# Kernel optimization log

Measured on AMD Instinct MI355X. Metric: run time of the kernel, lower is better.

The kernel has to match this reference:

```python
import jax, jax.numpy as jnp
import numpy as np

B, T, NE, NH, HD = 4, 1024, 768, 12, 64
CURV = 0.0
EPS = 1e-6
LN_EPS = 1e-5
ROPE_BASE = 10000.0


def project(x, k):
    # Lift Euclidean vector onto Lorentz hyperboloid with curvature K = exp(k):
    # time coord t = sqrt(K + ||x||^2) so that <lx, lx>_L = -K.
    K = jnp.exp(k)
    t = jnp.sqrt(K + jnp.sum(x * x, axis=-1, keepdims=True))
    return jnp.concatenate([t, x], axis=-1)


def lorentz_distance(lq, lk, k):
    # lq, lk: (B, H, T, D+1); k: (1, H, 1, 1) log-curvature.
    # d = sqrt(K) * arccosh(clamp(-<q,k>_L / K, 1+eps))
    K = jnp.exp(k)
    inner = (jnp.einsum('bhid,bhjd->bhij', lq[..., 1:], lk[..., 1:])
             - jnp.einsum('bhi,bhj->bhij', lq[..., 0], lk[..., 0]))
    c = jnp.clip(-inner / K, 1.0 + EPS, None)
    return jnp.sqrt(K) * jnp.arccosh(c)


def lorentz_norm(x):
    # sqrt(|<x,x>_L|) with <x,x>_L = -x0^2 + ||xs||^2  (keepdim)
    inner = -x[..., 0:1] ** 2 + jnp.sum(x[..., 1:] ** 2, axis=-1, keepdims=True)
    return jnp.sqrt(jnp.clip(-inner, EPS, None))


def rotary_tables():
    inv_freq = 1.0 / (ROPE_BASE ** (np.arange(0, HD, 2, dtype=np.float32) / HD))
    t = np.arange(T, dtype=np.float32)
    freqs = np.outer(t, inv_freq)  # (T, HD/2)
    cos = jnp.asarray(np.cos(freqs))[None, :, None, :]  # (1,T,1,HD/2)
    sin = jnp.asarray(np.sin(freqs))[None, :, None, :]
    return cos, sin


def apply_rotary(x, cos, sin):
    # x: (B, T, H, HD)
    x1, x2 = x[..., : HD // 2], x[..., HD // 2:]
    return jnp.concatenate([x1 * cos + x2 * sin, -x1 * sin + x2 * cos], axis=-1)


def layernorm(y, g, b):
    m = jnp.mean(y, axis=-1, keepdims=True)
    v = jnp.mean((y - m) ** 2, axis=-1, keepdims=True)
    return (y - m) / jnp.sqrt(v + LN_EPS) * g + b


def setup_inputs() -> dict:
    key = jax.random.key(0)
    ks = jax.random.split(key, 8)
    s = 0.02
    return {
        'x': jax.random.normal(ks[0], (B, T, NE), dtype=jnp.float32),
        'block_curvature': jnp.asarray(CURV, dtype=jnp.float32),
        'mlp_curvature': jnp.asarray(CURV, dtype=jnp.float32),
        'attn_curvatures': jnp.ones((1, NH, 1, 1), dtype=jnp.float32) * CURV,
        'qkv_w': jax.random.normal(ks[1], (3 * NE, NE + 1), dtype=jnp.float32) * s,
        'attn_proj_w': jax.random.normal(ks[2], (NE, (HD + 1) * NH), dtype=jnp.float32) * s,
        'attn_proj_b': jnp.zeros((NE,), dtype=jnp.float32),
        'mlp_expand_w': jax.random.normal(ks[3], (4 * NE + 3, NE + 1), dtype=jnp.float32) * s,
        'mlp_expand_b': jnp.zeros((4 * NE + 3,), dtype=jnp.float32),
        'mlp_shrink_w': jax.random.normal(ks[4], (NE, 4 * (NE + 1)), dtype=jnp.float32) * s,
        'mlp_shrink_b': jnp.zeros((NE,), dtype=jnp.float32),
        'ln_g': jnp.ones((NE,), dtype=jnp.float32),
        'ln_b': jnp.zeros((NE,), dtype=jnp.float32),
    }


def reference(x, block_curvature, mlp_curvature, attn_curvatures, qkv_w,
              attn_proj_w, attn_proj_b, mlp_expand_w, mlp_expand_b,
              mlp_shrink_w, mlp_shrink_b, ln_g, ln_b):
    cos, sin = rotary_tables()
    causal_bias = jnp.where(
        jnp.triu(jnp.ones((T, T), dtype=bool), k=1), -jnp.inf, 0.0).astype(jnp.float32)

    def block_norm(lx):
        return project(layernorm(lx[..., 1:], ln_g, ln_b), block_curvature)

    def attn(lx):
        qkv = lx @ qkv_w.T  # (B, T, 3*NE)
        q, k, v = jnp.split(qkv, 3, axis=-1)
        q = apply_rotary(q.reshape(B, T, NH, HD), cos, sin)
        k = apply_rotary(k.reshape(B, T, NH, HD), cos, sin)
        v = v.reshape(B, T, NH, HD)
        lq = project(q.transpose(0, 2, 1, 3), attn_curvatures)  # (B,H,T,HD+1)
        lk = project(k.transpose(0, 2, 1, 3), attn_curvatures)
        lv = project(v.transpose(0, 2, 1, 3), attn_curvatures)
        dis = lorentz_distance(lq, lk, attn_curvatures)  # (B,H,T,T)
        aw = jax.nn.softmax(-dis + causal_bias, axis=-1)
        a = jnp.einsum('bhij,bhjd->bhid', aw, lv)  # (B,H,T,HD+1)
        a = a * jnp.sqrt(jnp.exp(attn_curvatures)) / lorentz_norm(a)
        a = a.transpose(0, 2, 1, 3).reshape(B, T, NH * (HD + 1))
        a = a @ attn_proj_w.T + attn_proj_b
        return project(a, block_curvature)

    def mlp(lx):
        h = lx @ mlp_expand_w.T + mlp_expand_b  # (B,T,4*NE+3)
        h = project(h, mlp_curvature)[..., 1:]  # drop time coord back to 4*NE+3
        h = jax.nn.gelu(h, approximate=False)
        h = project(h, mlp_curvature)  # (B,T,4*(NE+1))
        h = h @ mlp_shrink_w.T + mlp_shrink_b
        return project(h, block_curvature)

    def skip(lx, f_lx):
        return project(lx[..., 1:] + f_lx[..., 1:], block_curvature)

    lx = project(x, block_curvature)  # (B,T,NE+1)
    lx = skip(lx, attn(block_norm(lx)))
    lx = skip(lx, mlp(block_norm(lx)))
    return lx
```

## Files before the change

### kernel.cpp

```cpp
#include <hip/hip_runtime.h>
#include <cmath>

typedef unsigned short ushort_t;
typedef __attribute__((ext_vector_type(8))) short short8;
typedef __attribute__((ext_vector_type(4))) float floatx4;

#define NH    12
#define T     1024
#define ROWS  4096
#define NE    768
#define KPA   832
#define KPB   3136
#define NEXP  3200
#define HEXP  3075
#define NSPLIT 3

__device__ __forceinline__ ushort_t f2bf(float f) {
  union { float f; unsigned u; } v; v.f = f;
  unsigned r = v.u + 0x7fffu + ((v.u >> 16) & 1u);
  return (ushort_t)(r >> 16);
}
__device__ __forceinline__ ushort_t f2bf_trunc(float f) {
  union { float f; unsigned u; } v; v.f = f;
  return (ushort_t)(v.u >> 16);
}
__device__ __forceinline__ float bf2f(ushort_t b) {
  union { unsigned u; float f; } v; v.u = ((unsigned)b) << 16;
  return v.f;
}
__device__ __forceinline__ float blk_reduce_sum(float v, float* sm) {
  #pragma unroll
  for (int o = 32; o > 0; o >>= 1) v += __shfl_xor(v, o, 64);
  int lane = threadIdx.x & 63, w = threadIdx.x >> 6;
  __syncthreads();
  if (lane == 0) sm[w] = v;
  __syncthreads();
  return sm[0] + sm[1] + sm[2] + sm[3];
}
__device__ __forceinline__ float red16_sum(float v) {
  #pragma unroll
  for (int o = 1; o < 16; o <<= 1) v += __shfl_xor(v, o, 64);
  return v;
}

#define NB_A 7488
#define NB_B 2496
#define NB_C 10400
#define NB_D 9408
#define NB_E 16
__device__ __forceinline__ void cvt_elem(ushort_t* __restrict__ dst,
                                         const float* __restrict__ src,
                                         int idx, int srcRows, int srcK, int dstK) {
  int r = idx / dstK, c = idx - r * dstK;
  dst[idx] = (r < srcRows && c < srcK) ? f2bf(src[(size_t)r * srcK + c]) : (ushort_t)0;
}
__global__ __launch_bounds__(256) void prep_kernel(
    ushort_t* __restrict__ qkv_wb, const float* __restrict__ qkvw,
    ushort_t* __restrict__ proj_wb, const float* __restrict__ projw,
    ushort_t* __restrict__ exp_wb, const float* __restrict__ expw,
    ushort_t* __restrict__ shr_wb, const float* __restrict__ shrw,
    ushort_t* __restrict__ aout_bf,
    const float* __restrict__ xin, const float* __restrict__ g,
    const float* __restrict__ bb, const float* __restrict__ curv,
    ushort_t* __restrict__ lnp) {
  __shared__ float sm[4];
  int blk = blockIdx.x;
  int tid = threadIdx.x;
  if (blk < NB_A) {
    cvt_elem(qkv_wb, qkvw, blk * 256 + tid, 2304, 769, KPA);
  } else if (blk < NB_A + NB_B) {
    cvt_elem(proj_wb, projw, (blk - NB_A) * 256 + tid, 768, 780, KPA);
  } else if (blk < NB_A + NB_B + NB_C) {
    cvt_elem(exp_wb, expw, (blk - NB_A - NB_B) * 256 + tid, HEXP, 769, KPA);
  } else if (blk < NB_A + NB_B + NB_C + NB_D) {
    cvt_elem(shr_wb, shrw, (blk - NB_A - NB_B - NB_C) * 256 + tid, 768, 3076, KPB);
  } else if (blk < NB_A + NB_B + NB_C + NB_D + NB_E) {
    int r = (blk - NB_A - NB_B - NB_C - NB_D) * 256 + tid;
    ushort_t* p = aout_bf + (size_t)r * KPA + 780;
    #pragma unroll
    for (int j = 0; j < KPA - 780; ++j) p[j] = 0;
  } else {
    const int row = blk - (NB_A + NB_B + NB_C + NB_D + NB_E);
    const float* xr = xin + (size_t)row * NE;
    float xv[3];
    float s = 0.f, ss = 0.f;
    #pragma unroll
    for (int i = 0; i < 3; ++i) {
      xv[i] = xr[tid + 256 * i];
      s += xv[i]; ss += xv[i] * xv[i];
    }
    s = blk_reduce_sum(s, sm);
    ss = blk_reduce_sum(ss, sm);
    float mean = s * (1.f / 768.f);
    float var = ss * (1.f / 768.f) - mean * mean;
    float rstd = rsqrtf(var + 1e-5f);
    float yv[3]; float ys = 0.f;
    #pragma unroll
    for (int i = 0; i < 3; ++i) {
      int c = tid + 256 * i;
      yv[i] = (xv[i] - mean) * rstd * g[c] + bb[c];
      ys += yv[i] * yv[i];
    }
    ys = blk_reduce_sum(ys, sm);
    float tc = sqrtf(expf(curv[0]) + ys);
    ushort_t* orow = lnp + (size_t)row * KPA;
    #pragma unroll
    for (int i = 0; i < 3; ++i) orow[1 + tid + 256 * i] = f2bf(yv[i]);
    if (tid == 0) orow[0] = f2bf(tc);
    if (tid < KPA - 769) orow[769 + tid] = 0;
  }
}

__global__ __launch_bounds__(256) void gemm_bf16(
    const ushort_t* __restrict__ A, int lda,
    const ushort_t* __restrict__ W, int ldw,
    void* __restrict__ Cout, int ldc,
    int nkTot, int cpt,
    const float* __restrict__ bias, int biasN,
    const float* __restrict__ res, int ldres,
    int outMode, void* __restrict__ Cp) {
  __shared__ ushort_t As[2][128 * 64];
  __shared__ ushort_t Bs[2][128 * 64];
  const int tid = threadIdx.x;
  const int w = tid >> 6, lane = tid & 63;
  const int rowBase = (int)blockIdx.y << 7;
  const int colBase = (int)blockIdx.x << 7;
  const int wm = (w & 1) * 64, wn = (w >> 1) * 64;
  const int lm = lane & 15, quad = lane >> 4;
  const int p0 = quad ^ (lm & 7);

  floatx4 acc[4][4];
  #pragma unroll
  for (int i = 0; i < 4; ++i)
    #pragma unroll
    for (int j = 0; j < 4; ++j) {
      floatx4 z = {0.f, 0.f, 0.f, 0.f};
      acc[i][j] = z;
    }

  const int kt0 = (int)blockIdx.z * cpt;
  const int kt1 = min(nkTot, kt0 + cpt);

  auto stage = [&](int kt, int bsel) {
    #pragma unroll
    for (int j = 0; j < 4; ++j) {
      int ci = j * 256 + tid;
      int r = ci >> 3;
      int g = (ci & 7) ^ (r & 7);
      const ushort_t* ga = A + (size_t)(rowBase + r) * lda + kt * 64 + g * 8;
      const ushort_t* gb = W + (size_t)(colBase + r) * ldw + kt * 64 + g * 8;
      __builtin_amdgcn_global_load_lds(
          (const __attribute__((address_space(1))) void*)ga,
          (__attribute__((address_space(3))) void*)&As[bsel][(j * 256 + w * 64) * 8],
          16, 0, 0);
      __builtin_amdgcn_global_load_lds(
          (const __attribute__((address_space(1))) void*)gb,
          (__attribute__((address_space(3))) void*)&Bs[bsel][(j * 256 + w * 64) * 8],
          16, 0, 0);
    }
  };

  stage(kt0, 0);
  asm volatile("s_waitcnt vmcnt(0)" ::: "memory");
  __builtin_amdgcn_s_barrier();
  __builtin_amdgcn_sched_barrier(0);

  int cur = 0;
  for (int kt = kt0; kt < kt1; ++kt) {
    const bool hasNext = (kt + 1 < kt1);
    if (hasNext) stage(kt + 1, cur ^ 1);

    #pragma unroll
    for (int s = 0; s < 2; ++s) {
      const int ps = s ? (p0 ^ 4) : p0;
      short8 af[4], bfr[4];
      #pragma unroll
      for (int i = 0; i < 4; ++i) {
        af[i]  = *(const short8*)&As[cur][(wm + i * 16 + lm) * 64 + ps * 8];
        bfr[i] = *(const short8*)&Bs[cur][(wn + i * 16 + lm) * 64 + ps * 8];
      }
      #pragma unroll
      for (int i = 0; i < 4; ++i)
        #pragma unroll
        for (int jn = 0; jn < 4; ++jn)
          acc[i][jn] = __builtin_amdgcn_mfma_f32_16x16x32_bf16(
              af[i], bfr[jn], acc[i][jn], 0, 0, 0);
    }

    if (hasNext) {
      asm volatile("s_waitcnt vmcnt(0)" ::: "memory");
      __builtin_amdgcn_s_barrier();
      __builtin_amdgcn_sched_barrier(0);
    }
    cur ^= 1;
  }

  if (gridDim.z > 1) {
    ushort_t* dst = (ushort_t*)Cp + (size_t)blockIdx.z * ROWS * ldc;
    #pragma unroll
    for (int i = 0; i < 4; ++i)
      #pragma unroll
      for (int jn = 0; jn < 4; ++jn) {
        const int col = colBase + wn + jn * 16 + lm;
        #pragma unroll
        for (int rg = 0; rg < 4; ++rg) {
          const int row = rowBase + wm + i * 16 + quad * 4 + rg;
          dst[(size_t)row * ldc + col] = f2bf(acc[i][jn][rg]);
        }
      }
  } else if (outMode == 1) {
    ushort_t* C = (ushort_t*)Cout;
    #pragma unroll
    for (int i = 0; i < 4; ++i)
      #pragma unroll
      for (int jn = 0; jn < 4; ++jn) {
        const int col = colBase + wn + jn * 16 + lm;
        const float bv = bias ? ((col < biasN) ? bias[col] : 0.f) : 0.f;
        #pragma unroll
        for (int rg = 0; rg < 4; ++rg) {
          const int row = rowBase + wm + i * 16 + quad * 4 + rg;
          C[(size_t)row * ldc + col] = f2bf(acc[i][jn][rg] + bv);
        }
      }
  } else {
    float* C = (float*)Cout;
    #pragma unroll
    for (int i = 0; i < 4; ++i)
      #pragma unroll
      for (int jn = 0; jn < 4; ++jn) {
        const int col = colBase + wn + jn * 16 + lm;
        const float bv = bias ? ((col < biasN) ? bias[col] : 0.f) : 0.f;
        #pragma unroll
        for (int rg = 0; rg < 4; ++rg) {
          const int row = rowBase + wm + i * 16 + quad * 4 + rg;
          float o = acc[i][jn][rg] + bv;
          if (res) o += res[(size_t)row * ldres + col];
          C[(size_t)row * ldc + col] = o;
        }
      }
  }
}

__global__ __launch_bounds__(256) void rope_project(
    const ushort_t* __restrict__ qkv, const float* __restrict__ ac,
    ushort_t* __restrict__ qb, ushort_t* __restrict__ kb, ushort_t* __restrict__ vtb,
    float* __restrict__ q0, float* __restrict__ k0, float* __restrict__ v0) {
  int gid = blockIdx.x * 4 + (threadIdx.x >> 6);
  int lane = threadIdx.x & 63;
  int h = gid % NH;
  int bt = gid / NH;
  int t = bt & (T - 1);
  int b = bt >> 10;
  size_t base = (size_t)bt * 2304 + h * 64;
  float qv = bf2f(qkv[base + lane]);
  float kv = bf2f(qkv[base + 768 + lane]);
  float vv = bf2f(qkv[base + 1536 + lane]);
  int f = lane & 31;
  float ang = (float)t * __builtin_amdgcn_exp2f(-(float)f * 0.4152410118661534f);
  float sn, cs;
  sincosf(ang, &sn, &cs);
  float qp = __shfl(qv, lane ^ 32, 64);
  float kp = __shfl(kv, lane ^ 32, 64);
  float qr = (lane < 32) ? (qv * cs + qp * sn) : (-qp * sn + qv * cs);
  float kr = (lane < 32) ? (kv * cs + kp * sn) : (-kp * sn + kv * cs);
  float Kh = expf(ac[h]);
  float sq = qr * qr, sk = kr * kr, sv = vv * vv;
  #pragma unroll
  for (int o = 32; o > 0; o >>= 1) {
    sq += __shfl_xor(sq, o, 64);
    sk += __shfl_xor(sk, o, 64);
    sv += __shfl_xor(sv, o, 64);
  }
  size_t idx = ((size_t)(b * NH + h) * T + t);
  qb[idx * 64 + lane] = f2bf(qr);
  kb[idx * 64 + lane] = f2bf(kr);
  vtb[(size_t)(b * NH + h) * (64 * T) + (size_t)lane * T + t] = f2bf(vv);
  if (lane == 0) {
    q0[idx] = sqrtf(Kh + sq);
    k0[idx] = sqrtf(Kh + sk);
    v0[idx] = sqrtf(Kh + sv);
  }
}

__global__ __launch_bounds__(512, 4) void attn_kernel(
    const ushort_t* __restrict__ qb, const ushort_t* __restrict__ kb,
    const ushort_t* __restrict__ vtb,
    const float* __restrict__ q0, const float* __restrict__ k0,
    const float* __restrict__ v0,
    const float* __restrict__ ac,
    ushort_t* __restrict__ Opart, float* __restrict__ lpart,
    float* __restrict__ a0part) {
  __shared__ ushort_t Qs[128 * 64];
  __shared__ ushort_t Ks[2][64 * 64];
  __shared__ ushort_t Vts[2][64 * 64];
  __shared__ ushort_t Ps[128 * 72];

  const int sIdx = blockIdx.x;
  const int qtile = (int)gridDim.y - 1 - (int)blockIdx.y;
  const int bh = blockIdx.z;
  const int h = bh % NH;
  const int qt0 = qtile * 128;
  const int tid = threadIdx.x;
  const int w = tid >> 6, lane = tid & 63;
  const int lm = lane & 15, quad = lane >> 4;
  const int wm = w * 16;
  const int sw = lm & 7;

  const int n = 2 * qtile + 2;
  const int kbeg = (n * sIdx) / NSPLIT;
  const int kend = (n * (sIdx + 1)) / NSPLIT;
  const size_t pb = (size_t)(sIdx * 48 + bh) * T;

  if (kbeg >= kend) {
    #pragma unroll
    for (int r = 0; r < 4; ++r) {
      const int i = qt0 + wm + quad * 4 + r;
      ushort_t* orow = Opart + (pb + i) * 64;
      #pragma unroll
      for (int nt = 0; nt < 4; ++nt) orow[nt * 16 + lm] = 0;
      if (lm == 0) { lpart[pb + i] = 0.f; a0part[pb + i] = 0.f; }
    }
    return;
  }

  const float Kh = expf(ac[h]);
  const float sqrtK = sqrtf(Kh);
  const float invK = 1.0f / Kh;
  const float nsK = -sqrtK;
  const bool k1 = (Kh == 1.0f);

  {
    const ushort_t* qtp = qb + ((size_t)bh * T + qt0) * 64;
    #pragma unroll
    for (int j = 0; j < 2; ++j) {
      int ci = j * 512 + tid;
      int r = ci >> 3;
      int clog = ((ci & 7) ^ (r & 7)) * 8;
      __builtin_amdgcn_global_load_lds(
          (const __attribute__((address_space(1))) void*)(qtp + r * 64 + clog),
          (__attribute__((address_space(3))) void*)&Qs[(j * 8 + w) * 512],
          16, 0, 0);
    }
  }
  const ushort_t* kbase = kb + (size_t)bh * T * 64;
  const ushort_t* vbh = vtb + (size_t)bh * (64 * T);
  const float* k0row = k0 + (size_t)bh * T;
  const float* v0row = v0 + (size_t)bh * T;
  const int ldr = tid >> 3;
  const int ldcs = ((tid & 7) ^ (ldr & 7)) * 8;
  {
    const int j0 = kbeg * 64;
    __builtin_amdgcn_global_load_lds(
        (const __attribute__((address_space(1))) void*)(kbase + (size_t)(j0 + ldr) * 64 + ldcs),
        (__attribute__((address_space(3))) void*)&Ks[0][w * 512], 16, 0, 0);
    __builtin_amdgcn_global_load_lds(
        (const __attribute__((address_space(1))) void*)(vbh + (size_t)ldr * T + j0 + ldcs),
        (__attribute__((address_space(3))) void*)&Vts[0][w * 512], 16, 0, 0);
  }
  float k0n[4], v0n[4];
  #pragma unroll
  for (int jt = 0; jt < 4; ++jt) {
    k0n[jt] = k0row[kbeg * 64 + jt * 16 + lm];
    v0n[jt] = v0row[kbeg * 64 + jt * 16 + lm];
  }
  float q0rv[4];
  #pragma unroll
  for (int r = 0; r < 4; ++r)
    q0rv[r] = q0[(size_t)bh * T + qt0 + wm + quad * 4 + r];

  asm volatile("s_waitcnt vmcnt(0)" ::: "memory");
  __builtin_amdgcn_s_barrier();
  __builtin_amdgcn_sched_barrier(0);

  const short8 qf0 = *(const short8*)&Qs[(wm + lm) * 64 + ((0 + quad) ^ sw) * 8];
  const short8 qf1 = *(const short8*)&Qs[(wm + lm) * 64 + ((4 + quad) ^ sw) * 8];

  float lsum[4], a0r[4];
  floatx4 oacc[4];
  #pragma unroll
  for (int r = 0; r < 4; ++r) { lsum[r] = 0.f; a0r[r] = 0.f; }
  #pragma unroll
  for (int nt = 0; nt < 4; ++nt) { floatx4 z = {0.f,0.f,0.f,0.f}; oacc[nt] = z; }

  int cur = 0;
  for (int kt = kbeg; kt < kend; ++kt) {
    const bool hasNext = (kt + 1 < kend);
    float k0i[4], v0v[4];
    #pragma unroll
    for (int jt = 0; jt < 4; ++jt) { k0i[jt] = k0n[jt] * invK; v0v[jt] = v0n[jt]; }

    if (hasNext) {
      const int j0n = (kt + 1) * 64;
      __builtin_amdgcn_global_load_lds(
          (const __attribute__((address_space(1))) void*)(kbase + (size_t)(j0n + ldr) * 64 + ldcs),
          (__attribute__((address_space(3))) void*)&Ks[cur ^ 1][w * 512], 16, 0, 0);
      __builtin_amdgcn_global_load_lds(
          (const __attribute__((address_space(1))) void*)(vbh + (size_t)ldr * T + j0n + ldcs),
          (__attribute__((address_space(3))) void*)&Vts[cur ^ 1][w * 512], 16, 0, 0);
      #pragma unroll
      for (int jt = 0; jt < 4; ++jt) {
        k0n[jt] = k0row[j0n + jt * 16 + lm];
        v0n[jt] = v0row[j0n + jt * 16 + lm];
      }
    }

    const int j0 = kt * 64;
    const ushort_t* Kc = Ks[cur];
    const ushort_t* Vc = Vts[cur];

    floatx4 sacc[4];
    #pragma unroll
    for (int jt = 0; jt < 4; ++jt) {
      const int krow = jt * 16 + lm;
      short8 kf0 = *(const short8*)&Kc[krow * 64 + ((0 + quad) ^ sw) * 8];
      short8 kf1 = *(const short8*)&Kc[krow * 64 + ((4 + quad) ^ sw) * 8];
      floatx4 z = {0.f, 0.f, 0.f, 0.f};
      z = __builtin_amdgcn_mfma_f32_16x16x32_bf16(qf0, kf0, z, 0, 0, 0);
      z = __builtin_amdgcn_mfma_f32_16x16x32_bf16(qf1, kf1, z, 0, 0, 0);
      sacc[jt] = z;
    }

    const bool maskT = (kt >= 2 * qtile);
    if (k1) {
      #pragma unroll
      for (int r = 0; r < 4; ++r) {
        const int i = qt0 + wm + quad * 4 + r;
        float ls = 0.f, a0s = 0.f;
        #pragma unroll
        for (int jt = 0; jt < 4; ++jt) {
          float c = fmaf(-invK, sacc[jt][r], q0rv[r] * k0i[jt]);
          c = fmaxf(c, 1.000001f);
          float p = c - sqrtf(fmaf(c, c, -1.f));
          if (maskT && (j0 + jt * 16 + lm > i)) p = 0.f;
          ushort_t pb2 = f2bf_trunc(p);
          Ps[(wm + quad * 4 + r) * 72 + jt * 16 + lm] = pb2;
          float pf = bf2f(pb2);
          ls += pf;
          a0s = fmaf(pf, v0v[jt], a0s);
        }
        lsum[r] += ls;
        a0r[r] += a0s;
      }
    } else {
      #pragma unroll
      for (int r = 0; r < 4; ++r) {
        const int i = qt0 + wm + quad * 4 + r;
        float ls = 0.f, a0s = 0.f;
        #pragma unroll
        for (int jt = 0; jt < 4; ++jt) {
          float c = fmaf(-invK, sacc[jt][r], q0rv[r] * k0i[jt]);
          c = fmaxf(c, 1.000001f);
          float z = c + sqrtf(fmaf(c, c, -1.f));
          float p = __builtin_amdgcn_exp2f(nsK * __builtin_amdgcn_logf(z));
          if (maskT && (j0 + jt * 16 + lm > i)) p = 0.f;
          ushort_t pb2 = f2bf_trunc(p);
          Ps[(wm + quad * 4 + r) * 72 + jt * 16 + lm] = pb2;
          float pf = bf2f(pb2);
          ls += pf;
          a0s = fmaf(pf, v0v[jt], a0s);
        }
        lsum[r] += ls;
        a0r[r] += a0s;
      }
    }

    short8 pf0 = *(const short8*)&Ps[(wm + lm) * 72 + quad * 8];
    short8 pf1 = *(const short8*)&Ps[(wm + lm) * 72 + 32 + quad * 8];
    #pragma unroll
    for (int nt = 0; nt < 4; ++nt) {
      const int vrow = nt * 16 + lm;
      short8 vf0 = *(const short8*)&Vc[vrow * 64 + ((0 + quad) ^ sw) * 8];
      short8 vf1 = *(const short8*)&Vc[vrow * 64 + ((4 + quad) ^ sw) * 8];
      oacc[nt] = __builtin_amdgcn_mfma_f32_16x16x32_bf16(pf0, vf0, oacc[nt], 0, 0, 0);
      oacc[nt] = __builtin_amdgcn_mfma_f32_16x16x32_bf16(pf1, vf1, oacc[nt], 0, 0, 0);
    }

    if (hasNext) {
      asm volatile("s_waitcnt vmcnt(0)" ::: "memory");
      __builtin_amdgcn_s_barrier();
      __builtin_amdgcn_sched_barrier(0);
    }
    cur ^= 1;
  }

  #pragma unroll
  for (int r = 0; r < 4; ++r) {
    float lf = red16_sum(lsum[r]);
    float a0f = red16_sum(a0r[r]);
    const int i = qt0 + wm + quad * 4 + r;
    ushort_t* orow = Opart + (pb + i) * 64;
    #pragma unroll
    for (int nt = 0; nt < 4; ++nt) orow[nt * 16 + lm] = f2bf(oacc[nt][r]);
    if (lm == 0) { lpart[pb + i] = lf; a0part[pb + i] = a0f; }
  }
}

__global__ __launch_bounds__(256) void attn_combine(
    const ushort_t* __restrict__ Opart, const float* __restrict__ lpart,
    const float* __restrict__ a0part,
    const float* __restrict__ ac, ushort_t* __restrict__ aout) {
  const int widx = blockIdx.x * 4 + (threadIdx.x >> 6);
  const int lane = threadIdx.x & 63;
  const int bh = widx >> 10;
  const int t = widx & 1023;
  const int h = bh % NH, b = bh / NH;
  float L = 0.f, A0 = 0.f, O = 0.f;
  #pragma unroll
  for (int sp = 0; sp < NSPLIT; ++sp) {
    const size_t r = (size_t)(sp * 48 + bh) * T + t;
    L += lpart[r];
    A0 += a0part[r];
    O += bf2f(Opart[r * 64 + lane]);
  }
  const float invl = 1.f / L;
  float av = O * invl;
  float ssq = av * av;
  #pragma unroll
  for (int o = 32; o > 0; o >>= 1) ssq += __shfl_xor(ssq, o, 64);
  float a0n = A0 * invl;
  float nsq = fmaxf(a0n * a0n - ssq, 1e-6f);
  float Kh = expf(ac[h]);
  float scale = sqrtf(Kh) * rsqrtf(nsq);
  ushort_t* orow = aout + (size_t)(b * T + t) * KPA + h * 65;
  orow[1 + lane] = f2bf(av * scale);
  if (lane == 0) orow[0] = f2bf(a0n * scale);
}

__global__ __launch_bounds__(256) void gelu_project(
    const ushort_t* __restrict__ hsrc, const float* __restrict__ curv,
    ushort_t* __restrict__ hp) {
  __shared__ float sm[4];
  const int row = blockIdx.x;
  const int tid = threadIdx.x;
  const ushort_t* hr = hsrc + (size_t)row * NEXP;
  float gv[13];
  float ss = 0.f;
  #pragma unroll
  for (int i = 0; i < 13; ++i) {
    int c = tid + 256 * i;
    float xx = (c < HEXP) ? bf2f(hr[c]) : 0.f;
    float gg = 0.5f * xx * (1.f + erff(xx * 0.70710678118654752f));
    gv[i] = gg; ss += gg * gg;
  }
  ss = blk_reduce_sum(ss, sm);
  float tc = sqrtf(expf(curv[0]) + ss);
  ushort_t* orow = hp + (size_t)row * KPB;
  #pragma unroll
  for (int i = 0; i < 13; ++i) {
    int c = tid + 256 * i;
    if (c < HEXP) orow[1 + c] = f2bf(gv[i]);
  }
  if (tid == 0) orow[0] = f2bf(tc);
  if (tid < KPB - (HEXP + 1)) orow[HEXP + 1 + tid] = 0;
}

__global__ __launch_bounds__(256) void reduce_ln_project(
    const ushort_t* __restrict__ Cp, int nsplit,
    const float* __restrict__ bias, const float* __restrict__ res,
    float* __restrict__ x2out,
    const float* __restrict__ g, const float* __restrict__ bb,
    const float* __restrict__ curv, ushort_t* __restrict__ lnp) {
  __shared__ float sm[4];
  const int row = blockIdx.x;
  const int tid = threadIdx.x;
  float xv[3];
  float s = 0.f, ss = 0.f;
  #pragma unroll
  for (int i = 0; i < 3; ++i) {
    const int c = tid + 256 * i;
    float v = bias[c] + res[(size_t)row * NE + c];
    for (int sp = 0; sp < nsplit; ++sp)
      v += bf2f(Cp[(size_t)sp * ROWS * NE + (size_t)row * NE + c]);
    x2out[(size_t)row * NE + c] = v;
    xv[i] = v;
    s += v; ss += v * v;
  }
  s = blk_reduce_sum(s, sm);
  ss = blk_reduce_sum(ss, sm);
  float mean = s * (1.f / 768.f);
  float var = ss * (1.f / 768.f) - mean * mean;
  float rstd = rsqrtf(var + 1e-5f);
  float yv[3]; float ys = 0.f;
  #pragma unroll
  for (int i = 0; i < 3; ++i) {
    int c = tid + 256 * i;
    yv[i] = (xv[i] - mean) * rstd * g[c] + bb[c];
    ys += yv[i] * yv[i];
  }
  ys = blk_reduce_sum(ys, sm);
  float tc = sqrtf(expf(curv[0]) + ys);
  ushort_t* orow = lnp + (size_t)row * KPA;
  #pragma unroll
  for (int i = 0; i < 3; ++i) orow[1 + tid + 256 * i] = f2bf(yv[i]);
  if (tid == 0) orow[0] = f2bf(tc);
  if (tid < KPA - 769) orow[769 + tid] = 0;
}

__global__ __launch_bounds__(256) void reduce_final_project(
    const ushort_t* __restrict__ Cp, int nsplit,
    const float* __restrict__ bias, const float* __restrict__ res,
    const float* __restrict__ curv, float* __restrict__ out) {
  __shared__ float sm[4];
  const int row = blockIdx.x;
  const int tid = threadIdx.x;
  float v[3]; float ss = 0.f;
  #pragma unroll
  for (int i = 0; i < 3; ++i) {
    const int c = tid + 256 * i;
    float t = bias[c] + res[(size_t)row * NE + c];
    for (int sp = 0; sp < nsplit; ++sp)
      t += bf2f(Cp[(size_t)sp * ROWS * NE + (size_t)row * NE + c]);
    v[i] = t; ss += t * t;
  }
  ss = blk_reduce_sum(ss, sm);
  float tc = sqrtf(expf(curv[0]) + ss);
  float* o = out + (size_t)row * 769;
  #pragma unroll
  for (int i = 0; i < 3; ++i) o[1 + tid + 256 * i] = v[i];
  if (tid == 0) o[0] = tc;
}

extern "C" void kernel_launch(void* const* d_in, const int* in_sizes, int n_in,
                              void* d_out, int out_size, void* d_ws, size_t ws_size,
                              hipStream_t stream) {
  (void)in_sizes; (void)n_in; (void)out_size; (void)ws_size;
  const float* x     = (const float*)d_in[0];
  const float* bc    = (const float*)d_in[1];
  const float* mc    = (const float*)d_in[2];
  const float* ac    = (const float*)d_in[3];
  const float* qkvw  = (const float*)d_in[4];
  const float* projw = (const float*)d_in[5];
  const float* projb = (const float*)d_in[6];
  const float* expw  = (const float*)d_in[7];
  const float* expb  = (const float*)d_in[8];
  const float* shrw  = (const float*)d_in[9];
  const float* shrb  = (const float*)d_in[10];
  const float* lng   = (const float*)d_in[11];
  const float* lnb   = (const float*)d_in[12];
  float* out = (float*)d_out;

  float* x2 = (float*)d_ws;
  ushort_t* qkv_wb  = (ushort_t*)(x2 + (size_t)ROWS * NE);
  ushort_t* proj_wb = qkv_wb + (size_t)2304 * KPA;
  ushort_t* exp_wb  = proj_wb + (size_t)768 * KPA;
  ushort_t* shr_wb  = exp_wb + (size_t)NEXP * KPA;
  ushort_t* lnp_bf  = shr_wb + (size_t)768 * KPB;
  ushort_t* aout_bf = lnp_bf + (size_t)ROWS * KPA;
  char* r2 = (char*)(aout_bf + (size_t)ROWS * KPA);
  ushort_t* qkvb = (ushort_t*)r2;
  ushort_t* qbb = qkvb + (size_t)ROWS * 2304;
  ushort_t* kbb = qbb + (size_t)48 * T * 64;
  ushort_t* vtb = kbb + (size_t)48 * T * 64;
  float* q0b = (float*)(vtb + (size_t)48 * T * 64);
  float* k0b = q0b + (size_t)48 * T;
  float* v0b = k0b + (size_t)48 * T;
  ushort_t* Opart = (ushort_t*)(v0b + (size_t)48 * T);
  float* lpart = (float*)(Opart + (size_t)NSPLIT * 48 * T * 64);
  float* a0part = lpart + (size_t)NSPLIT * 48 * T;
  ushort_t* ppartP = (ushort_t*)r2;
  ushort_t* hbbf = (ushort_t*)r2;
  ushort_t* hp_bf = hbbf + (size_t)ROWS * NEXP;
  ushort_t* ppartS = hp_bf + (size_t)ROWS * KPB;

  prep_kernel<<<NB_A + NB_B + NB_C + NB_D + NB_E + ROWS, 256, 0, stream>>>(
      qkv_wb, qkvw, proj_wb, projw, exp_wb, expw, shr_wb, shrw, aout_bf,
      x, lng, lnb, bc, lnp_bf);
  gemm_bf16<<<dim3(2304 / 128, ROWS / 128, 1), 256, 0, stream>>>(
      lnp_bf, KPA, qkv_wb, KPA, qkvb, 2304, KPA / 64, KPA / 64,
      nullptr, 0, nullptr, 0, 1, nullptr);
  rope_project<<<(ROWS * NH) / 4, 256, 0, stream>>>(qkvb, ac, qbb, kbb, vtb, q0b, k0b, v0b);
  attn_kernel<<<dim3(NSPLIT, T / 128, 48), 512, 0, stream>>>(
      qbb, kbb, vtb, q0b, k0b, v0b, ac, Opart, lpart, a0part);
  attn_combine<<<(48 * T) / 4, 256, 0, stream>>>(Opart, lpart, a0part, ac, aout_bf);
  gemm_bf16<<<dim3(768 / 128, ROWS / 128, 2), 256, 0, stream>>>(
      aout_bf, KPA, proj_wb, KPA, nullptr, NE, KPA / 64, 7,
      nullptr, 0, nullptr, 0, 0, ppartP);
  reduce_ln_project<<<ROWS, 256, 0, stream>>>(
      ppartP, 2, projb, x, x2, lng, lnb, bc, lnp_bf);
  gemm_bf16<<<dim3(NEXP / 128, ROWS / 128, 1), 256, 0, stream>>>(
      lnp_bf, KPA, exp_wb, KPA, hbbf, NEXP, KPA / 64, KPA / 64,
      expb, HEXP, nullptr, 0, 1, nullptr);
  gelu_project<<<ROWS, 256, 0, stream>>>(hbbf, mc, hp_bf);
  gemm_bf16<<<dim3(768 / 128, ROWS / 128, 4), 256, 0, stream>>>(
      hp_bf, KPB, shr_wb, KPB, nullptr, NE, KPB / 64, 13,
      nullptr, 0, nullptr, 0, 0, ppartS);
  reduce_final_project<<<ROWS, 256, 0, stream>>>(
      ppartS, 4, shrb, x2, bc, out);
}
```

Baseline: 381.5 us.

## Fuse GELU and row sum-of-squares into expand GEMM epilogue; single-buffer GEMM LDS

```diff
diff --git a/kernel.cpp b/kernel.cpp
--- a/kernel.cpp
+++ b/kernel.cpp
@@ -118,13 +118,26 @@
     int nkTot, int cpt,
     const float* __restrict__ bias, int biasN,
     const float* __restrict__ res, int ldres,
-    int outMode, void* __restrict__ Cp) {
-  __shared__ ushort_t As[2][128 * 64];
-  __shared__ ushort_t Bs[2][128 * 64];
+    int outMode, void* __restrict__ Cp,
+    float* __restrict__ ssacc) {
+  __shared__ ushort_t As[128 * 64];
+  __shared__ ushort_t Bs[128 * 64];
   const int tid = threadIdx.x;
   const int w = tid >> 6, lane = tid & 63;
-  const int rowBase = (int)blockIdx.y << 7;
-  const int colBase = (int)blockIdx.x << 7;
+
+  int bx = blockIdx.x, by = blockIdx.y;
+  {
+    const int gx = gridDim.x, gy = gridDim.y;
+    const int nwg = gx * gy;
+    if ((nwg & 7) == 0) {
+      int lin = by * gx + bx;
+      int swz = (lin & 7) * (nwg >> 3) + (lin >> 3);
+      bx = swz % gx;
+      by = swz / gx;
+    }
+  }
+  const int rowBase = by << 7;
+  const int colBase = bx << 7;
   const int wm = (w & 1) * 64, wn = (w >> 1) * 64;
   const int lm = lane & 15, quad = lane >> 4;
   const int p0 = quad ^ (lm & 7);
@@ -140,8 +153,8 @@
 
   const int kt0 = (int)blockIdx.z * cpt;
   const int kt1 = min(nkTot, kt0 + cpt);
-
-  auto stage = [&](int kt, int bsel) {
+  for (int kt = kt0; kt < kt1; ++kt) {
+    __syncthreads();
     #pragma unroll
     for (int j = 0; j < 4; ++j) {
       int ci = j * 256 + tid;
@@ -151,24 +164,14 @@
       const ushort_t* gb = W + (size_t)(colBase + r) * ldw + kt * 64 + g * 8;
       __builtin_amdgcn_global_load_lds(
           (const __attribute__((address_space(1))) void*)ga,
-          (__attribute__((address_space(3))) void*)&As[bsel][(j * 256 + w * 64) * 8],
+          (__attribute__((address_space(3))) void*)&As[(j * 256 + w * 64) * 8],
           16, 0, 0);
       __builtin_amdgcn_global_load_lds(
           (const __attribute__((address_space(1))) void*)gb,
-          (__attribute__((address_space(3))) void*)&Bs[bsel][(j * 256 + w * 64) * 8],
+          (__attribute__((address_space(3))) void*)&Bs[(j * 256 + w * 64) * 8],
           16, 0, 0);
     }
-  };
-
-  stage(kt0, 0);
-  asm volatile("s_waitcnt vmcnt(0)" ::: "memory");
-  __builtin_amdgcn_s_barrier();
-  __builtin_amdgcn_sched_barrier(0);
-
-  int cur = 0;
-  for (int kt = kt0; kt < kt1; ++kt) {
-    const bool hasNext = (kt + 1 < kt1);
-    if (hasNext) stage(kt + 1, cur ^ 1);
+    __syncthreads();
 
     #pragma unroll
     for (int s = 0; s < 2; ++s) {
@@ -176,8 +179,8 @@
       short8 af[4], bfr[4];
       #pragma unroll
       for (int i = 0; i < 4; ++i) {
-        af[i]  = *(const short8*)&As[cur][(wm + i * 16 + lm) * 64 + ps * 8];
-        bfr[i] = *(const short8*)&Bs[cur][(wn + i * 16 + lm) * 64 + ps * 8];
+        af[i]  = *(const short8*)&As[(wm + i * 16 + lm) * 64 + ps * 8];
+        bfr[i] = *(const short8*)&Bs[(wn + i * 16 + lm) * 64 + ps * 8];
       }
       #pragma unroll
       for (int i = 0; i < 4; ++i)
@@ -186,13 +189,6 @@
           acc[i][jn] = __builtin_amdgcn_mfma_f32_16x16x32_bf16(
               af[i], bfr[jn], acc[i][jn], 0, 0, 0);
     }
-
-    if (hasNext) {
-      asm volatile("s_waitcnt vmcnt(0)" ::: "memory");
-      __builtin_amdgcn_s_barrier();
-      __builtin_amdgcn_sched_barrier(0);
-    }
-    cur ^= 1;
   }
 
   if (gridDim.z > 1) {
@@ -222,6 +218,38 @@
           C[(size_t)row * ldc + col] = f2bf(acc[i][jn][rg] + bv);
         }
       }
+  } else if (outMode == 2) {
+    ushort_t* C = (ushort_t*)Cout;
+    #pragma unroll
+    for (int i = 0; i < 4; ++i) {
+      float ssq[4] = {0.f, 0.f, 0.f, 0.f};
+      #pragma unroll
+      for (int jn = 0; jn < 4; ++jn) {
+        const int col = colBase + wn + jn * 16 + lm;
+        const bool valid = col < biasN;
+        const float bv = valid ? bias[col] : 0.f;
+        #pragma unroll
+        for (int rg = 0; rg < 4; ++rg) {
+          const int row = rowBase + wm + i * 16 + quad * 4 + rg;
+          float xx = acc[i][jn][rg] + bv;
+          float gg = 0.5f * xx * (1.f + erff(xx * 0.70710678118654752f));
+          if (valid) {
+            C[(size_t)row * ldc + 1 + col] = f2bf(gg);
+            ssq[rg] += gg * gg;
+          }
+        }
+      }
+      #pragma unroll
+      for (int rg = 0; rg < 4; ++rg) {
+        float s2 = ssq[rg];
+        #pragma unroll
+        for (int o = 1; o < 16; o <<= 1) s2 += __shfl_xor(s2, o, 64);
+        if (lm == 0) {
+          const int row = rowBase + wm + i * 16 + quad * 4 + rg;
+          atomicAdd(&ssacc[row], s2);
+        }
+      }
+    }
   } else {
     float* C = (float*)Cout;
     #pragma unroll
@@ -526,32 +554,14 @@
   if (lane == 0) orow[0] = f2bf(a0n * scale);
 }
 
-__global__ __launch_bounds__(256) void gelu_project(
-    const ushort_t* __restrict__ hsrc, const float* __restrict__ curv,
+__global__ __launch_bounds__(256) void hp_finalize(
+    const float* __restrict__ ssacc, const float* __restrict__ curv,
     ushort_t* __restrict__ hp) {
-  __shared__ float sm[4];
-  const int row = blockIdx.x;
-  const int tid = threadIdx.x;
-  const ushort_t* hr = hsrc + (size_t)row * NEXP;
-  float gv[13];
-  float ss = 0.f;
-  #pragma unroll
-  for (int i = 0; i < 13; ++i) {
-    int c = tid + 256 * i;
-    float xx = (c < HEXP) ? bf2f(hr[c]) : 0.f;
-    float gg = 0.5f * xx * (1.f + erff(xx * 0.70710678118654752f));
-    gv[i] = gg; ss += gg * gg;
-  }
-  ss = blk_reduce_sum(ss, sm);
-  float tc = sqrtf(expf(curv[0]) + ss);
+  const int row = blockIdx.x * 4 + (threadIdx.x >> 6);
+  const int lane = threadIdx.x & 63;
   ushort_t* orow = hp + (size_t)row * KPB;
-  #pragma unroll
-  for (int i = 0; i < 13; ++i) {
-    int c = tid + 256 * i;
-    if (c < HEXP) orow[1 + c] = f2bf(gv[i]);
-  }
-  if (tid == 0) orow[0] = f2bf(tc);
-  if (tid < KPB - (HEXP + 1)) orow[HEXP + 1 + tid] = 0;
+  if (lane == 0) orow[0] = f2bf(sqrtf(expf(curv[0]) + ssacc[row]));
+  if (lane < KPB - (HEXP + 1)) orow[HEXP + 1 + lane] = 0;
 }
 
 __global__ __launch_bounds__(256) void reduce_ln_project(
@@ -559,10 +569,12 @@
     const float* __restrict__ bias, const float* __restrict__ res,
     float* __restrict__ x2out,
     const float* __restrict__ g, const float* __restrict__ bb,
-    const float* __restrict__ curv, ushort_t* __restrict__ lnp) {
+    const float* __restrict__ curv, ushort_t* __restrict__ lnp,
+    float* __restrict__ ssz) {
   __shared__ float sm[4];
   const int row = blockIdx.x;
   const int tid = threadIdx.x;
+  if (tid == 0) ssz[row] = 0.f;
   float xv[3];
   float s = 0.f, ss = 0.f;
   #pragma unroll
@@ -646,7 +658,8 @@
   ushort_t* shr_wb  = exp_wb + (size_t)NEXP * KPA;
   ushort_t* lnp_bf  = shr_wb + (size_t)768 * KPB;
   ushort_t* aout_bf = lnp_bf + (size_t)ROWS * KPA;
-  char* r2 = (char*)(aout_bf + (size_t)ROWS * KPA);
+  float* ssacc = (float*)(aout_bf + (size_t)ROWS * KPA);
+  char* r2 = (char*)(ssacc + ROWS);
   ushort_t* qkvb = (ushort_t*)r2;
   ushort_t* qbb = qkvb + (size_t)ROWS * 2304;
   ushort_t* kbb = qbb + (size_t)48 * T * 64;
@@ -658,8 +671,7 @@
   float* lpart = (float*)(Opart + (size_t)NSPLIT * 48 * T * 64);
   float* a0part = lpart + (size_t)NSPLIT * 48 * T;
   ushort_t* ppartP = (ushort_t*)r2;
-  ushort_t* hbbf = (ushort_t*)r2;
-  ushort_t* hp_bf = hbbf + (size_t)ROWS * NEXP;
+  ushort_t* hp_bf = (ushort_t*)r2;
   ushort_t* ppartS = hp_bf + (size_t)ROWS * KPB;
 
   prep_kernel<<<NB_A + NB_B + NB_C + NB_D + NB_E + ROWS, 256, 0, stream>>>(
@@ -667,23 +679,23 @@
       x, lng, lnb, bc, lnp_bf);
   gemm_bf16<<<dim3(2304 / 128, ROWS / 128, 1), 256, 0, stream>>>(
       lnp_bf, KPA, qkv_wb, KPA, qkvb, 2304, KPA / 64, KPA / 64,
-      nullptr, 0, nullptr, 0, 1, nullptr);
+      nullptr, 0, nullptr, 0, 1, nullptr, nullptr);
   rope_project<<<(ROWS * NH) / 4, 256, 0, stream>>>(qkvb, ac, qbb, kbb, vtb, q0b, k0b, v0b);
   attn_kernel<<<dim3(NSPLIT, T / 128, 48), 512, 0, stream>>>(
       qbb, kbb, vtb, q0b, k0b, v0b, ac, Opart, lpart, a0part);
   attn_combine<<<(48 * T) / 4, 256, 0, stream>>>(Opart, lpart, a0part, ac, aout_bf);
   gemm_bf16<<<dim3(768 / 128, ROWS / 128, 2), 256, 0, stream>>>(
       aout_bf, KPA, proj_wb, KPA, nullptr, NE, KPA / 64, 7,
-      nullptr, 0, nullptr, 0, 0, ppartP);
+      nullptr, 0, nullptr, 0, 0, ppartP, nullptr);
   reduce_ln_project<<<ROWS, 256, 0, stream>>>(
-      ppartP, 2, projb, x, x2, lng, lnb, bc, lnp_bf);
+      ppartP, 2, projb, x, x2, lng, lnb, bc, lnp_bf, ssacc);
   gemm_bf16<<<dim3(NEXP / 128, ROWS / 128, 1), 256, 0, stream>>>(
-      lnp_bf, KPA, exp_wb, KPA, hbbf, NEXP, KPA / 64, KPA / 64,
-      expb, HEXP, nullptr, 0, 1, nullptr);
-  gelu_project<<<ROWS, 256, 0, stream>>>(hbbf, mc, hp_bf);
+      lnp_bf, KPA, exp_wb, KPA, hp_bf, KPB, KPA / 64, KPA / 64,
+      expb, HEXP, nullptr, 0, 2, nullptr, ssacc);
+  hp_finalize<<<ROWS / 4, 256, 0, stream>>>(ssacc, mc, hp_bf);
   gemm_bf16<<<dim3(768 / 128, ROWS / 128, 4), 256, 0, stream>>>(
       hp_bf, KPB, shr_wb, KPB, nullptr, NE, KPB / 64, 13,
-      nullptr, 0, nullptr, 0, 0, ppartS);
+      nullptr, 0, nullptr, 0, 0, ppartS, nullptr);
   reduce_final_project<<<ROWS, 256, 0, stream>>>(
       ppartS, 4, shrb, x2, bc, out);
 }
```

Result: no change. 377.2 us (-1.1%).

## Single-buffer GEMM LDS tiles and add XCD-aware workgroup index swizzle

Applied to the files above, without the earlier changes.

```diff
diff --git a/kernel.cpp b/kernel.cpp
--- a/kernel.cpp
+++ b/kernel.cpp
@@ -119,12 +119,24 @@
     const float* __restrict__ bias, int biasN,
     const float* __restrict__ res, int ldres,
     int outMode, void* __restrict__ Cp) {
-  __shared__ ushort_t As[2][128 * 64];
-  __shared__ ushort_t Bs[2][128 * 64];
+  __shared__ ushort_t As[128 * 64];
+  __shared__ ushort_t Bs[128 * 64];
   const int tid = threadIdx.x;
   const int w = tid >> 6, lane = tid & 63;
-  const int rowBase = (int)blockIdx.y << 7;
-  const int colBase = (int)blockIdx.x << 7;
+
+  int bx = blockIdx.x, by = blockIdx.y;
+  {
+    const int gx = gridDim.x, gy = gridDim.y;
+    const int nwg = gx * gy;
+    if ((nwg & 7) == 0) {
+      int lin = by * gx + bx;
+      int swz = (lin & 7) * (nwg >> 3) + (lin >> 3);
+      bx = swz % gx;
+      by = swz / gx;
+    }
+  }
+  const int rowBase = by << 7;
+  const int colBase = bx << 7;
   const int wm = (w & 1) * 64, wn = (w >> 1) * 64;
   const int lm = lane & 15, quad = lane >> 4;
   const int p0 = quad ^ (lm & 7);
@@ -140,8 +152,8 @@
 
   const int kt0 = (int)blockIdx.z * cpt;
   const int kt1 = min(nkTot, kt0 + cpt);
-
-  auto stage = [&](int kt, int bsel) {
+  for (int kt = kt0; kt < kt1; ++kt) {
+    __syncthreads();
     #pragma unroll
     for (int j = 0; j < 4; ++j) {
       int ci = j * 256 + tid;
@@ -151,24 +163,14 @@
       const ushort_t* gb = W + (size_t)(colBase + r) * ldw + kt * 64 + g * 8;
       __builtin_amdgcn_global_load_lds(
           (const __attribute__((address_space(1))) void*)ga,
-          (__attribute__((address_space(3))) void*)&As[bsel][(j * 256 + w * 64) * 8],
+          (__attribute__((address_space(3))) void*)&As[(j * 256 + w * 64) * 8],
           16, 0, 0);
       __builtin_amdgcn_global_load_lds(
           (const __attribute__((address_space(1))) void*)gb,
-          (__attribute__((address_space(3))) void*)&Bs[bsel][(j * 256 + w * 64) * 8],
+          (__attribute__((address_space(3))) void*)&Bs[(j * 256 + w * 64) * 8],
           16, 0, 0);
     }
-  };
-
-  stage(kt0, 0);
-  asm volatile("s_waitcnt vmcnt(0)" ::: "memory");
-  __builtin_amdgcn_s_barrier();
-  __builtin_amdgcn_sched_barrier(0);
-
-  int cur = 0;
-  for (int kt = kt0; kt < kt1; ++kt) {
-    const bool hasNext = (kt + 1 < kt1);
-    if (hasNext) stage(kt + 1, cur ^ 1);
+    __syncthreads();
 
     #pragma unroll
     for (int s = 0; s < 2; ++s) {
@@ -176,8 +178,8 @@
       short8 af[4], bfr[4];
       #pragma unroll
       for (int i = 0; i < 4; ++i) {
-        af[i]  = *(const short8*)&As[cur][(wm + i * 16 + lm) * 64 + ps * 8];
-        bfr[i] = *(const short8*)&Bs[cur][(wn + i * 16 + lm) * 64 + ps * 8];
+        af[i]  = *(const short8*)&As[(wm + i * 16 + lm) * 64 + ps * 8];
+        bfr[i] = *(const short8*)&Bs[(wn + i * 16 + lm) * 64 + ps * 8];
       }
       #pragma unroll
       for (int i = 0; i < 4; ++i)
@@ -186,13 +188,6 @@
           acc[i][jn] = __builtin_amdgcn_mfma_f32_16x16x32_bf16(
               af[i], bfr[jn], acc[i][jn], 0, 0, 0);
     }
-
-    if (hasNext) {
-      asm volatile("s_waitcnt vmcnt(0)" ::: "memory");
-      __builtin_amdgcn_s_barrier();
-      __builtin_amdgcn_sched_barrier(0);
-    }
-    cur ^= 1;
   }
 
   if (gridDim.z > 1) {
```

New measurement: 370.0 us. 1.03x faster.
